# Optimization experiments

Hardware: AMD Instinct MI355X
Metric: run time of the kernel (lower is better)

Reference implementation:

```python
import jax, jax.numpy as jnp
import numpy as np

B, T, D_IN, D_OUT = 4, 2048, 1024, 1024


def setup_inputs() -> dict:
    key = jax.random.key(0)
    k1, k2, k3, k4 = jax.random.split(key, 4)
    s_in = 1.0 / np.sqrt(D_IN)
    return {
        "input_vector": jax.random.normal(k1, (B, T, D_IN), dtype=jnp.float32),
        "w_q": jax.random.normal(k2, (D_IN, D_OUT), dtype=jnp.float32) * s_in,
        "w_k": jax.random.normal(k3, (D_IN, D_OUT), dtype=jnp.float32) * s_in,
        "w_v": jax.random.normal(k4, (D_IN, D_OUT), dtype=jnp.float32) * s_in,
    }


def reference(input_vector, w_q, w_k, w_v):
    # projections: [B, T, D_OUT]
    q = jnp.einsum("btd,de->bte", input_vector, w_q)
    k = jnp.einsum("btd,de->bte", input_vector, w_k)
    v = jnp.einsum("btd,de->bte", input_vector, w_v)

    T_ = q.shape[1]
    # raw scores [B, T, T]
    scores = jnp.einsum("bqd,bkd->bqk", q, k)
    # causal mask (strict upper triangle masked to -inf), applied BEFORE scaling
    # (as in the original; -inf is invariant under the scale anyway)
    causal = jnp.tril(jnp.ones((T_, T_), dtype=bool))  # True = keep
    scores = jnp.where(causal[None, :, :], scores, -jnp.inf)
    scores = scores / jnp.sqrt(jnp.asarray(k.shape[-1], scores.dtype))
    attn = jax.nn.softmax(scores, axis=-1)
    # dropout = 0.0 (eval): identity
    return jnp.einsum("bqk,bkd->bqd", attn, v)
```

## Files before the change

### kernel.cpp

```cpp
#include <hip/hip_runtime.h>
#include <cstdint>

typedef unsigned short u16;
typedef __attribute__((ext_vector_type(8))) short short8;
typedef __attribute__((ext_vector_type(16))) float f32x16;

__device__ __forceinline__ u16 f2bf(float f) {
  uint32_t u = __float_as_uint(f);
  u += 0x7FFFu + ((u >> 16) & 1u);
  return (u16)(u >> 16);
}

__device__ __forceinline__ void async_ld16(u16* lds, const u16* g) {
  __builtin_amdgcn_global_load_lds((const __attribute__((address_space(1))) uint32_t*)g,
                                   (__attribute__((address_space(3))) uint32_t*)lds,
                                   16, 0, 0);
}

__device__ __forceinline__ void lgkm0_fence() {
  asm volatile("s_waitcnt lgkmcnt(0)" ::: "memory");
  __builtin_amdgcn_sched_barrier(0);
}
#define VM_FENCE(N) do { asm volatile("s_waitcnt vmcnt(" #N ")" ::: "memory"); \
                         __builtin_amdgcn_sched_barrier(0); } while (0)

#define MFMA32 __builtin_amdgcn_mfma_f32_32x32x16_bf16

template <int ROLE>
__global__ __launch_bounds__(512, 2) void g8(
    const u16* __restrict__ Xbf, const u16* __restrict__ Wt,
    u16* __restrict__ QK, u16* __restrict__ VtAll,
    u16* __restrict__ P, float* __restrict__ lpart)
{
  const int b = blockIdx.x;
  const int tid = threadIdx.x;
  const int lane = tid & 63;
  const int wave = tid >> 6;
  const int wr2 = wave >> 2;
  const int wc2 = wave & 3;
  const int m32 = lane & 31;
  const int hh = lane >> 5;

  __shared__ __align__(16) u16 ls[2][2][16384];

  const u16 *Abase, *Brow0, *Brow1;
  int m0, n0, zb = 0;
  bool vthalf = false;

  if constexpr (ROLE == 0) {
    if (b < 256) {
      m0 = (b >> 3) * 256;
      n0 = (b & 7) * 128;
      Abase = Xbf;
      Brow0 = Wt + (long)(n0)*1024;
      Brow1 = Wt + 1024L * 1024 + (long)(n0)*1024;
    } else {
      vthalf = true;
      const int v = b - 256;
      m0 = (v >> 5) * 128;
      n0 = (v & 31) * 256;
      Abase = Wt + 2L * 1024 * 1024;
      Brow0 = Xbf + (long)(n0)*1024;
      Brow1 = Xbf + (long)(n0 + 128) * 1024;
    }
  } else {
    zb = b / 36;
    const int w = b - zb * 36;
    int mt = 0;
    while ((mt + 1) * (mt + 2) / 2 <= w) ++mt;
    const int nt = w - mt * (mt + 1) / 2;
    m0 = nt * 256;
    n0 = mt * 256;
    Abase = QK + 8192L * 1024 + (long)zb * 2048 * 1024;
    const u16* Bq = QK + (long)zb * 2048 * 1024;
    Brow0 = Bq + (long)(n0)*1024;
    Brow1 = Bq + (long)(n0 + 128) * 1024;
  }

  const int sr = tid >> 3, sg = tid & 7;
  const long swz = (long)((sg ^ (sr & 7)) * 8);
  const u16* pAst = Abase + (long)(m0 + sr) * 1024 + swz;
  const u16* pB[2] = { Brow0 + (long)sr * 1024 + swz,
                       Brow1 + (long)sr * 1024 + swz };

#define STG_A(bf, h, t_) do { \
    u16* _d = &ls[bf][0][(h) * 8192] + tid * 8; \
    const u16* _s = pAst + (long)(h) * 131072 + (long)(t_) * 64; \
    async_ld16(_d, _s); async_ld16(_d + 4096, _s + 65536); } while (0)
#define STG_B(bf, h, t_) do { \
    u16* _d = &ls[bf][1][(h) * 8192] + tid * 8; \
    const u16* _s = pB[h] + (long)(t_) * 64; \
    async_ld16(_d, _s); async_ld16(_d + 4096, _s + 65536); } while (0)

  const int ec = lane & 31;
  const int rb = hh * 4;

  if constexpr (ROLE == 0) {
    if (vthalf) {
      int offAv[4], offBv[2][4];
#pragma unroll
      for (int ks = 0; ks < 4; ++ks) {
        const int kq = ((ks << 1) | hh) ^ (m32 & 7);
        offAv[ks] = (wr2 * 64 + m32) * 64 + kq * 8;
#pragma unroll
        for (int j = 0; j < 2; ++j)
          offBv[j][ks] = (wc2 * 64 + j * 32 + m32) * 64 + kq * 8;
      }

      f32x16 acc[2][2];
#pragma unroll
      for (int i = 0; i < 2; ++i)
#pragma unroll
        for (int j = 0; j < 2; ++j)
#pragma unroll
          for (int r = 0; r < 16; ++r) acc[i][j][r] = 0.f;

      STG_A(0, 0, 0); STG_B(0, 0, 0); STG_B(0, 1, 0);
      VM_FENCE(0);
      __builtin_amdgcn_s_barrier();

      short8 A0[4], A1[4], B0r[4], B1r[4];

#pragma unroll 1
      for (int t = 0; t < 16; ++t) {
        const u16* la = ls[t & 1][0];
        const u16* lb = ls[t & 1][1];
        const int nb = (t & 1) ^ 1;

#pragma unroll
        for (int ks = 0; ks < 4; ++ks) {
          A0[ks]  = *(const short8*)&la[offAv[ks]];
          A1[ks]  = *(const short8*)&la[offAv[ks] + 2048];
          B0r[ks] = *(const short8*)&lb[offBv[0][ks]];
        }
        if (t < 15) { STG_A(nb, 0, t + 1); STG_B(nb, 0, t + 1); }
        __builtin_amdgcn_s_barrier();
        lgkm0_fence();
        __builtin_amdgcn_s_setprio(1);
#pragma unroll
        for (int ks = 0; ks < 4; ++ks) {
          acc[0][0] = MFMA32(A0[ks], B0r[ks], acc[0][0], 0, 0, 0);
          acc[1][0] = MFMA32(A1[ks], B0r[ks], acc[1][0], 0, 0, 0);
        }
        __builtin_amdgcn_s_setprio(0);
        if (t < 15) VM_FENCE(4); else VM_FENCE(0);
        __builtin_amdgcn_s_barrier();

#pragma unroll
        for (int ks = 0; ks < 4; ++ks)
          B1r[ks] = *(const short8*)&lb[offBv[1][ks]];
        if (t < 15) STG_B(nb, 1, t + 1);
        __builtin_amdgcn_s_barrier();
        lgkm0_fence();
        __builtin_amdgcn_s_setprio(1);
#pragma unroll
        for (int ks = 0; ks < 4; ++ks) {
          acc[0][1] = MFMA32(A0[ks], B1r[ks], acc[0][1], 0, 0, 0);
          acc[1][1] = MFMA32(A1[ks], B1r[ks], acc[1][1], 0, 0, 0);
        }
        __builtin_amdgcn_s_setprio(0);
        if (t < 15) VM_FENCE(2); else VM_FENCE(0);
        __builtin_amdgcn_s_barrier();
      }

#pragma unroll
      for (int i = 0; i < 2; ++i) {
        const int rbase = m0 + wr2 * 64 + i * 32 + rb;
#pragma unroll
        for (int j = 0; j < 2; ++j) {
          const int col = n0 + wc2 * 64 + j * 32 + ec;
#pragma unroll
          for (int r = 0; r < 16; ++r) {
            const int row = rbase + (r & 3) + 8 * (r >> 2);
            VtAll[(long)row * 8192 + col] = f2bf(acc[i][j][r]);
          }
        }
      }
      return;
    }
  }

  int offAk[4], offBk[2][4];
#pragma unroll
  for (int ks = 0; ks < 4; ++ks) {
    const int kq = ((ks << 1) | hh) ^ (m32 & 7);
    offAk[ks] = (wr2 * 128 + m32) * 64 + kq * 8;
#pragma unroll
    for (int j = 0; j < 2; ++j) {
      const int rowB = (ROLE == 0) ? (j * 128 + wc2 * 32 + m32)
                                   : (wc2 * 64 + j * 32 + m32);
      offBk[j][ks] = rowB * 64 + kq * 8;
    }
  }

  f32x16 acc[4][2];
#pragma unroll
  for (int i = 0; i < 4; ++i)
#pragma unroll
    for (int j = 0; j < 2; ++j)
#pragma unroll
      for (int r = 0; r < 16; ++r) acc[i][j][r] = 0.f;

  STG_A(0, 0, 0); STG_A(0, 1, 0); STG_B(0, 0, 0); STG_B(0, 1, 0);
  STG_B(1, 0, 1); STG_B(1, 1, 1); STG_A(1, 0, 1);
  VM_FENCE(6);
  __builtin_amdgcn_s_barrier();

  short8 A0[4], A1[4], A2[4], A3[4], B0r[4], B1r[4];

#pragma unroll 1
  for (int t = 0; t < 16; ++t) {
    const u16* la = ls[t & 1][0];
    const u16* lb = ls[t & 1][1];

#pragma unroll
    for (int ks = 0; ks < 4; ++ks) {
      A0[ks]  = *(const short8*)&la[offAk[ks]];
      A1[ks]  = *(const short8*)&la[offAk[ks] + 2048];
      B0r[ks] = *(const short8*)&lb[offBk[0][ks]];
    }
    if (t < 15) STG_A((t + 1) & 1, 1, t + 1);
    __builtin_amdgcn_s_barrier();
    lgkm0_fence();
    __builtin_amdgcn_s_setprio(1);
#pragma unroll
    for (int ks = 0; ks < 4; ++ks) {
      acc[0][0] = MFMA32(A0[ks], B0r[ks], acc[0][0], 0, 0, 0);
      acc[1][0] = MFMA32(A1[ks], B0r[ks], acc[1][0], 0, 0, 0);
    }
    __builtin_amdgcn_s_setprio(0);
    __builtin_amdgcn_s_barrier();

#pragma unroll
    for (int ks = 0; ks < 4; ++ks)
      B1r[ks] = *(const short8*)&lb[offBk[1][ks]];
    __builtin_amdgcn_s_barrier();
    lgkm0_fence();
    __builtin_amdgcn_s_setprio(1);
#pragma unroll
    for (int ks = 0; ks < 4; ++ks) {
      acc[0][1] = MFMA32(A0[ks], B1r[ks], acc[0][1], 0, 0, 0);
      acc[1][1] = MFMA32(A1[ks], B1r[ks], acc[1][1], 0, 0, 0);
    }
    __builtin_amdgcn_s_setprio(0);
    __builtin_amdgcn_s_barrier();

#pragma unroll
    for (int ks = 0; ks < 4; ++ks) {
      A2[ks] = *(const short8*)&la[offAk[ks] + 4096];
      A3[ks] = *(const short8*)&la[offAk[ks] + 6144];
    }
    if (t < 14) STG_B(t & 1, 0, t + 2);
    __builtin_amdgcn_s_barrier();
    lgkm0_fence();
    __builtin_amdgcn_s_setprio(1);
#pragma unroll
    for (int ks = 0; ks < 4; ++ks) {
      acc[2][0] = MFMA32(A2[ks], B0r[ks], acc[2][0], 0, 0, 0);
      acc[3][0] = MFMA32(A3[ks], B0r[ks], acc[3][0], 0, 0, 0);
    }
    __builtin_amdgcn_s_setprio(0);
    __builtin_amdgcn_s_barrier();

    if (t < 14) { STG_B(t & 1, 1, t + 2); STG_A(t & 1, 0, t + 2); }
    __builtin_amdgcn_s_barrier();
    __builtin_amdgcn_s_setprio(1);
#pragma unroll
    for (int ks = 0; ks < 4; ++ks) {
      acc[2][1] = MFMA32(A2[ks], B1r[ks], acc[2][1], 0, 0, 0);
      acc[3][1] = MFMA32(A3[ks], B1r[ks], acc[3][1], 0, 0, 0);
    }
    __builtin_amdgcn_s_setprio(0);
    if (t < 14) VM_FENCE(6); else VM_FENCE(0);
    __builtin_amdgcn_s_barrier();
  }
#undef STG_A
#undef STG_B

  if constexpr (ROLE == 0) {
#pragma unroll
    for (int j = 0; j < 2; ++j) {
      u16* Cj = QK + (long)j * 8192 * 1024;
      const int col = n0 + wc2 * 32 + ec;
#pragma unroll
      for (int i = 0; i < 4; ++i) {
        const int rbase = m0 + wr2 * 128 + i * 32 + rb;
#pragma unroll
        for (int r = 0; r < 16; ++r) {
          const int row = rbase + (r & 3) + 8 * (r >> 2);
          Cj[(long)row * 1024 + col] = f2bf(acc[i][j][r]);
        }
      }
    }
  } else {
    u16* Pp = P + (long)zb * 2048 * 2048;
    float* lpz = lpart + (long)zb * 16 * 2048;
    const int chunk = (m0 >> 7) + wr2;
#pragma unroll
    for (int j = 0; j < 2; ++j) {
      const int q = n0 + wc2 * 64 + j * 32 + ec;
      float s = 0.f;
#pragma unroll
      for (int i = 0; i < 4; ++i) {
        const int kb = m0 + wr2 * 128 + i * 32 + rb;
#pragma unroll
        for (int u = 0; u < 4; ++u) {
          const int k0r = kb + u * 8;
          float pv4[4];
#pragma unroll
          for (int v = 0; v < 4; ++v) {
            float e = __expf(acc[i][j][u * 4 + v] * 0.03125f);
            if (k0r + v > q) e = 0.f;
            pv4[v] = e;
            s += e;
          }
          ushort4 o;
          o.x = f2bf(pv4[0]); o.y = f2bf(pv4[1]);
          o.z = f2bf(pv4[2]); o.w = f2bf(pv4[3]);
          *(ushort4*)&Pp[(long)q * 2048 + k0r] = o;
        }
      }
      s += __shfl_xor(s, 32, 64);
      if (hh == 0) lpz[(long)chunk * 2048 + q] = s;
    }
  }
}

__global__ __launch_bounds__(256) void pv(
    const u16* __restrict__ VtAll, const u16* __restrict__ P,
    const float* __restrict__ lpart, float* __restrict__ out)
{
  const int b = blockIdx.x;
  const int tid = threadIdx.x;
  const int lane = tid & 63;
  const int wave = tid >> 6;
  const int wm = wave >> 1;
  const int wn = wave & 1;
  const int m32 = lane & 31;
  const int hh = lane >> 5;

  __shared__ __align__(16) u16 lsa[2][8192];
  __shared__ __align__(16) u16 lsb[2][8192];
  __shared__ float l_s[128];

  const int id = b & 255;
  const int zb = id >> 6;
  const int r2 = id & 63;
  const int dn = r2 >> 3;
  const int pp = r2 & 7;
  const int qt = (b < 256) ? (15 - pp) : pp;
  const int m0 = qt * 128;
  const int n0 = dn * 128;
  const int nkt = (qt + 1) * 2;

  const u16* Ab = P + (long)zb * 2048 * 2048;
  const u16* Bb = VtAll + (long)zb * 2048;

  const int prow = tid >> 3;
  const long pswz = (long)(((tid & 7) ^ (prow & 7)) * 8);
  const u16* pA = Ab + (long)(m0 + prow) * 2048 + pswz;
  const u16* pB = Bb + (long)(n0 + prow) * 8192 + pswz;

#define PV_STG(bf, t_) do { \
    _Pragma("unroll") \
    for (int jj = 0; jj < 4; ++jj) { \
      async_ld16(&lsa[bf][(tid + jj * 256) * 8], pA + (long)jj * 32 * 2048 + (long)(t_) * 64); \
      async_ld16(&lsb[bf][(tid + jj * 256) * 8], pB + (long)jj * 32 * 8192 + (long)(t_) * 64); \
    } } while (0)

  int offA[2][4], offB[2][4];
#pragma unroll
  for (int ks = 0; ks < 4; ++ks) {
    const int kq = ((ks << 1) | hh) ^ (m32 & 7);
#pragma unroll
    for (int i = 0; i < 2; ++i) {
      offA[i][ks] = (wm * 64 + i * 32 + m32) * 64 + kq * 8;
      offB[i][ks] = (wn * 64 + i * 32 + m32) * 64 + kq * 8;
    }
  }

  f32x16 acc[2][2];
#pragma unroll
  for (int i = 0; i < 2; ++i)
#pragma unroll
    for (int j = 0; j < 2; ++j)
#pragma unroll
      for (int r = 0; r < 16; ++r) acc[i][j][r] = 0.f;

  PV_STG(0, 0);

#pragma unroll 1
  for (int t = 0; t < nkt; ++t) {
    __syncthreads();
    if (t + 1 < nkt) PV_STG((t & 1) ^ 1, t + 1);
    const u16* la = lsa[t & 1];
    const u16* lb = lsb[t & 1];
#pragma unroll
    for (int ks = 0; ks < 4; ++ks) {
      const short8 a0 = *(const short8*)&la[offA[0][ks]];
      const short8 a1 = *(const short8*)&la[offA[1][ks]];
      const short8 b0 = *(const short8*)&lb[offB[0][ks]];
      const short8 b1 = *(const short8*)&lb[offB[1][ks]];
      acc[0][0] = MFMA32(a0, b0, acc[0][0], 0, 0, 0);
      acc[0][1] = MFMA32(a0, b1, acc[0][1], 0, 0, 0);
      acc[1][0] = MFMA32(a1, b0, acc[1][0], 0, 0, 0);
      acc[1][1] = MFMA32(a1, b1, acc[1][1], 0, 0, 0);
    }
  }
#undef PV_STG

  __syncthreads();
  if (tid < 128) {
    const float* lp = lpart + (long)zb * 16 * 2048 + m0 + tid;
    float s = 0.f;
    for (int c = 0; c <= qt; ++c) s += lp[(long)c * 2048];
    l_s[tid] = 1.f / s;
  }
  __syncthreads();

  const int ec = lane & 31;
  const int rb = hh * 4;
  float* Cf = out + (long)zb * 2048 * 1024;
#pragma unroll
  for (int i = 0; i < 2; ++i) {
    const int rbl = wm * 64 + i * 32 + rb;
#pragma unroll
    for (int j = 0; j < 2; ++j) {
      const int col = n0 + wn * 64 + j * 32 + ec;
#pragma unroll
      for (int r = 0; r < 16; ++r) {
        const int rl = rbl + (r & 3) + 8 * (r >> 2);
        Cf[(long)(m0 + rl) * 1024 + col] = acc[i][j][r] * l_s[rl];
      }
    }
  }
}

__global__ __launch_bounds__(256) void cast_fused(
    const float* __restrict__ x, const float* __restrict__ w0,
    const float* __restrict__ w1, const float* __restrict__ w2,
    u16* __restrict__ Xbf, u16* __restrict__ Wt)
{
  const int b = blockIdx.x;
  if (b < 8192) {
    const long i = ((long)b * 256 + threadIdx.x) * 4;
    const float4 v = *(const float4*)(x + i);
    ushort4 o;
    o.x = f2bf(v.x); o.y = f2bf(v.y); o.z = f2bf(v.z); o.w = f2bf(v.w);
    *(ushort4*)(Xbf + i) = o;
  } else {
    const int bb = b - 8192;
    const int z = bb >> 10, rem = bb & 1023;
    const float* W = (z == 0) ? w0 : (z == 1) ? w1 : w2;
    u16* o = Wt + (long)z * 1024 * 1024;
    __shared__ float t[32][33];
    const int n0 = (rem & 31) * 32, k0 = (rem >> 5) * 32;
    const int tx = threadIdx.x & 31, ty = threadIdx.x >> 5;
    for (int r = ty; r < 32; r += 8) t[r][tx] = W[(long)(k0 + r) * 1024 + n0 + tx];
    __syncthreads();
    for (int r = ty; r < 32; r += 8) o[(long)(n0 + r) * 1024 + k0 + tx] = f2bf(t[tx][r]);
  }
}

extern "C" void kernel_launch(void* const* d_in, const int* in_sizes, int n_in,
                              void* d_out, int out_size, void* d_ws, size_t ws_size,
                              hipStream_t stream) {
  const float* X  = (const float*)d_in[0];
  const float* Wq = (const float*)d_in[1];
  const float* Wk = (const float*)d_in[2];
  const float* Wv = (const float*)d_in[3];
  float* out = (float*)d_out;

  u16* Xbf   = (u16*)d_ws;
  u16* Wt    = Xbf + 8192L * 1024;
  u16* QK    = Wt + 3L * 1024 * 1024;
  u16* VtAll = QK + 2L * 8192 * 1024;
  u16* P     = VtAll + 1024L * 8192;
  float* lpart = (float*)(P + 4L * 2048 * 2048);

  cast_fused<<<8192 + 3072, 256, 0, stream>>>(X, Wq, Wk, Wv, Xbf, Wt);

  g8<0><<<512, 512, 0, stream>>>(Xbf, Wt, QK, VtAll, P, lpart);

  g8<1><<<144, 512, 0, stream>>>(Xbf, Wt, QK, VtAll, P, lpart);

  pv<<<512, 256, 0, stream>>>(VtAll, P, lpart, out);
}
```

Before: 228.0 us.

## Deepen PV kernel pipeline to four-stage K=32 buffering with explicit waits

New measurement: 239.1 us. +4.9%, slower.

```diff
diff --git a/kernel.cpp b/kernel.cpp
--- a/kernel.cpp
+++ b/kernel.cpp
@@ -339,43 +339,46 @@
   const int m32 = lane & 31;
   const int hh = lane >> 5;
 
-  __shared__ __align__(16) u16 lsa[2][8192];
-  __shared__ __align__(16) u16 lsb[2][8192];
+  __shared__ __align__(16) u16 lsa[4][4096];
+  __shared__ __align__(16) u16 lsb[4][4096];
   __shared__ float l_s[128];
 
-  const int id = b & 255;
-  const int zb = id >> 6;
-  const int r2 = id & 63;
-  const int dn = r2 >> 3;
-  const int pp = r2 & 7;
-  const int qt = (b < 256) ? (15 - pp) : pp;
+  const int dn = b >> 6;
+  const int g  = b & 63;
+  const int zb = g >> 4;
+  const int qq = g & 15;
+  const int qt = (qq < 8) ? qq : 23 - qq;
   const int m0 = qt * 128;
   const int n0 = dn * 128;
-  const int nkt = (qt + 1) * 2;
+  const int nkt = (qt + 1) * 4;
 
   const u16* Ab = P + (long)zb * 2048 * 2048;
   const u16* Bb = VtAll + (long)zb * 2048;
 
-  const int prow = tid >> 3;
-  const long pswz = (long)(((tid & 7) ^ (prow & 7)) * 8);
-  const u16* pA = Ab + (long)(m0 + prow) * 2048 + pswz;
-  const u16* pB = Bb + (long)(n0 + prow) * 8192 + pswz;
+  const int c0 = tid, c1 = tid + 256;
+  const int r0 = c0 >> 2, q0 = ((c0 & 3) ^ ((c0 >> 3) & 3)) * 8;
+  const int r1 = c1 >> 2, q1 = ((c1 & 3) ^ ((c1 >> 3) & 3)) * 8;
+
+  const u16* pA0 = Ab + (long)(m0 + r0) * 2048 + q0;
+  const u16* pA1 = Ab + (long)(m0 + r1) * 2048 + q1;
+  const u16* pB0 = Bb + (long)(n0 + r0) * 8192 + q0;
+  const u16* pB1 = Bb + (long)(n0 + r1) * 8192 + q1;
 
 #define PV_STG(bf, t_) do { \
-    _Pragma("unroll") \
-    for (int jj = 0; jj < 4; ++jj) { \
-      async_ld16(&lsa[bf][(tid + jj * 256) * 8], pA + (long)jj * 32 * 2048 + (long)(t_) * 64); \
-      async_ld16(&lsb[bf][(tid + jj * 256) * 8], pB + (long)jj * 32 * 8192 + (long)(t_) * 64); \
-    } } while (0)
-
-  int offA[2][4], offB[2][4];
-#pragma unroll
-  for (int ks = 0; ks < 4; ++ks) {
-    const int kq = ((ks << 1) | hh) ^ (m32 & 7);
+    async_ld16(&lsa[bf][c0 * 8], pA0 + (long)(t_) * 32); \
+    async_ld16(&lsa[bf][c1 * 8], pA1 + (long)(t_) * 32); \
+    async_ld16(&lsb[bf][c0 * 8], pB0 + (long)(t_) * 32); \
+    async_ld16(&lsb[bf][c1 * 8], pB1 + (long)(t_) * 32); } while (0)
+
+  const int rsw = (m32 >> 1) & 3;
+  int offA[2][2], offB[2][2];
+#pragma unroll
+  for (int ks = 0; ks < 2; ++ks) {
+    const int kq = ((ks << 1) | hh) ^ rsw;
 #pragma unroll
     for (int i = 0; i < 2; ++i) {
-      offA[i][ks] = (wm * 64 + i * 32 + m32) * 64 + kq * 8;
-      offB[i][ks] = (wn * 64 + i * 32 + m32) * 64 + kq * 8;
+      offA[i][ks] = (wm * 64 + i * 32 + m32) * 32 + kq * 8;
+      offB[i][ks] = (wn * 64 + i * 32 + m32) * 32 + kq * 8;
     }
   }
 
@@ -387,29 +390,39 @@
 #pragma unroll
       for (int r = 0; r < 16; ++r) acc[i][j][r] = 0.f;
 
-  PV_STG(0, 0);
+  PV_STG(0, 0); PV_STG(1, 1); PV_STG(2, 2);
 
 #pragma unroll 1
   for (int t = 0; t < nkt; ++t) {
-    __syncthreads();
-    if (t + 1 < nkt) PV_STG((t & 1) ^ 1, t + 1);
-    const u16* la = lsa[t & 1];
-    const u16* lb = lsb[t & 1];
-#pragma unroll
-    for (int ks = 0; ks < 4; ++ks) {
-      const short8 a0 = *(const short8*)&la[offA[0][ks]];
-      const short8 a1 = *(const short8*)&la[offA[1][ks]];
-      const short8 b0 = *(const short8*)&lb[offB[0][ks]];
-      const short8 b1 = *(const short8*)&lb[offB[1][ks]];
-      acc[0][0] = MFMA32(a0, b0, acc[0][0], 0, 0, 0);
-      acc[0][1] = MFMA32(a0, b1, acc[0][1], 0, 0, 0);
-      acc[1][0] = MFMA32(a1, b0, acc[1][0], 0, 0, 0);
-      acc[1][1] = MFMA32(a1, b1, acc[1][1], 0, 0, 0);
-    }
+    if (t < nkt - 2)       VM_FENCE(8);
+    else if (t == nkt - 2) VM_FENCE(4);
+    else                   VM_FENCE(0);
+    __builtin_amdgcn_s_barrier();
+    if (t + 3 < nkt) PV_STG((t + 3) & 3, t + 3);
+
+    const u16* la = lsa[t & 3];
+    const u16* lb = lsb[t & 3];
+    short8 a0[2], a1[2], b0[2], b1[2];
+#pragma unroll
+    for (int ks = 0; ks < 2; ++ks) {
+      a0[ks] = *(const short8*)&la[offA[0][ks]];
+      a1[ks] = *(const short8*)&la[offA[1][ks]];
+      b0[ks] = *(const short8*)&lb[offB[0][ks]];
+      b1[ks] = *(const short8*)&lb[offB[1][ks]];
+    }
+    lgkm0_fence();
+    __builtin_amdgcn_s_setprio(1);
+#pragma unroll
+    for (int ks = 0; ks < 2; ++ks) {
+      acc[0][0] = MFMA32(a0[ks], b0[ks], acc[0][0], 0, 0, 0);
+      acc[0][1] = MFMA32(a0[ks], b1[ks], acc[0][1], 0, 0, 0);
+      acc[1][0] = MFMA32(a1[ks], b0[ks], acc[1][0], 0, 0, 0);
+      acc[1][1] = MFMA32(a1[ks], b1[ks], acc[1][1], 0, 0, 0);
+    }
+    __builtin_amdgcn_s_setprio(0);
   }
 #undef PV_STG
 
-  __syncthreads();
   if (tid < 128) {
     const float* lp = lpart + (long)zb * 16 * 2048 + m0 + tid;
     float s = 0.f;
```

## Widen PV kernel to 512 threads and reorder block-to-tile mapping

Applied to the files above, without the earlier changes.

Result: no change. 229.2 us (+0.5%).

```diff
diff --git a/kernel.cpp b/kernel.cpp
--- a/kernel.cpp
+++ b/kernel.cpp
@@ -326,7 +326,7 @@
   }
 }
 
-__global__ __launch_bounds__(256) void pv(
+__global__ __launch_bounds__(512, 4) void pv(
     const u16* __restrict__ VtAll, const u16* __restrict__ P,
     const float* __restrict__ lpart, float* __restrict__ out)
 {
@@ -334,8 +334,8 @@
   const int tid = threadIdx.x;
   const int lane = tid & 63;
   const int wave = tid >> 6;
-  const int wm = wave >> 1;
-  const int wn = wave & 1;
+  const int wm = wave >> 2;
+  const int wn = wave & 3;
   const int m32 = lane & 31;
   const int hh = lane >> 5;
 
@@ -343,12 +343,11 @@
   __shared__ __align__(16) u16 lsb[2][8192];
   __shared__ float l_s[128];
 
-  const int id = b & 255;
-  const int zb = id >> 6;
-  const int r2 = id & 63;
-  const int dn = r2 >> 3;
-  const int pp = r2 & 7;
-  const int qt = (b < 256) ? (15 - pp) : pp;
+  const int dn = b >> 6;
+  const int g  = b & 63;
+  const int zb = g >> 4;
+  const int qq = g & 15;
+  const int qt = (qq < 8) ? qq : 23 - qq;
   const int m0 = qt * 128;
   const int n0 = dn * 128;
   const int nkt = (qt + 1) * 2;
@@ -362,30 +361,26 @@
   const u16* pB = Bb + (long)(n0 + prow) * 8192 + pswz;
 
 #define PV_STG(bf, t_) do { \
-    _Pragma("unroll") \
-    for (int jj = 0; jj < 4; ++jj) { \
-      async_ld16(&lsa[bf][(tid + jj * 256) * 8], pA + (long)jj * 32 * 2048 + (long)(t_) * 64); \
-      async_ld16(&lsb[bf][(tid + jj * 256) * 8], pB + (long)jj * 32 * 8192 + (long)(t_) * 64); \
-    } } while (0)
-
-  int offA[2][4], offB[2][4];
+    async_ld16(&lsa[bf][tid * 8],         pA + (long)(t_) * 64); \
+    async_ld16(&lsa[bf][(tid + 512) * 8], pA + 64L * 2048 + (long)(t_) * 64); \
+    async_ld16(&lsb[bf][tid * 8],         pB + (long)(t_) * 64); \
+    async_ld16(&lsb[bf][(tid + 512) * 8], pB + 64L * 8192 + (long)(t_) * 64); } while (0)
+
+  int offA[2][4], offB[4];
 #pragma unroll
   for (int ks = 0; ks < 4; ++ks) {
     const int kq = ((ks << 1) | hh) ^ (m32 & 7);
 #pragma unroll
-    for (int i = 0; i < 2; ++i) {
+    for (int i = 0; i < 2; ++i)
       offA[i][ks] = (wm * 64 + i * 32 + m32) * 64 + kq * 8;
-      offB[i][ks] = (wn * 64 + i * 32 + m32) * 64 + kq * 8;
-    }
-  }
-
-  f32x16 acc[2][2];
+    offB[ks] = (wn * 32 + m32) * 64 + kq * 8;
+  }
+
+  f32x16 acc[2];
 #pragma unroll
   for (int i = 0; i < 2; ++i)
 #pragma unroll
-    for (int j = 0; j < 2; ++j)
-#pragma unroll
-      for (int r = 0; r < 16; ++r) acc[i][j][r] = 0.f;
+    for (int r = 0; r < 16; ++r) acc[i][r] = 0.f;
 
   PV_STG(0, 0);
 
@@ -399,12 +394,9 @@
     for (int ks = 0; ks < 4; ++ks) {
       const short8 a0 = *(const short8*)&la[offA[0][ks]];
       const short8 a1 = *(const short8*)&la[offA[1][ks]];
-      const short8 b0 = *(const short8*)&lb[offB[0][ks]];
-      const short8 b1 = *(const short8*)&lb[offB[1][ks]];
-      acc[0][0] = MFMA32(a0, b0, acc[0][0], 0, 0, 0);
-      acc[0][1] = MFMA32(a0, b1, acc[0][1], 0, 0, 0);
-      acc[1][0] = MFMA32(a1, b0, acc[1][0], 0, 0, 0);
-      acc[1][1] = MFMA32(a1, b1, acc[1][1], 0, 0, 0);
+      const short8 bb = *(const short8*)&lb[offB[ks]];
+      acc[0] = MFMA32(a0, bb, acc[0], 0, 0, 0);
+      acc[1] = MFMA32(a1, bb, acc[1], 0, 0, 0);
     }
   }
 #undef PV_STG
@@ -421,17 +413,14 @@
   const int ec = lane & 31;
   const int rb = hh * 4;
   float* Cf = out + (long)zb * 2048 * 1024;
+  const int col = n0 + wn * 32 + ec;
 #pragma unroll
   for (int i = 0; i < 2; ++i) {
     const int rbl = wm * 64 + i * 32 + rb;
 #pragma unroll
-    for (int j = 0; j < 2; ++j) {
-      const int col = n0 + wn * 64 + j * 32 + ec;
-#pragma unroll
-      for (int r = 0; r < 16; ++r) {
-        const int rl = rbl + (r & 3) + 8 * (r >> 2);
-        Cf[(long)(m0 + rl) * 1024 + col] = acc[i][j][r] * l_s[rl];
-      }
+    for (int r = 0; r < 16; ++r) {
+      const int rl = rbl + (r & 3) + 8 * (r >> 2);
+      Cf[(long)(m0 + rl) * 1024 + col] = acc[i][r] * l_s[rl];
     }
   }
 }
@@ -484,5 +473,5 @@
 
   g8<1><<<144, 512, 0, stream>>>(Xbf, Wt, QK, VtAll, P, lpart);
 
-  pv<<<512, 256, 0, stream>>>(VtAll, P, lpart, out);
-}
+  pv<<<512, 512, 0, stream>>>(VtAll, P, lpart, out);
+}
```
